# Kernel tuning notes

Measured on AMD Instinct MI355X. Metric: run time of the kernel, lower is better.

The kernel has to match this reference:

```python
import jax, jax.numpy as jnp
import numpy as np

EMBED_DIM = 1024
NUM_HEADS = 16
HEAD_DIM = EMBED_DIM // NUM_HEADS
LN_EPS = 1e-5


def setup_inputs() -> dict:
    key = jax.random.key(0)
    ks = jax.random.split(key, 5)
    N, L, C = 32, 577, EMBED_DIM
    x = jax.random.normal(ks[0], (N, L, C), dtype=jnp.float32)
    ln1_g = jnp.ones((C,), dtype=jnp.float32)
    ln1_b = jnp.zeros((C,), dtype=jnp.float32)
    w_in = jax.random.normal(ks[1], (3 * C, C), dtype=jnp.float32) * (C ** -0.5)
    b_in = jax.random.normal(ks[2], (3 * C,), dtype=jnp.float32) * 0.02
    w_out = jax.random.normal(ks[3], (C, C), dtype=jnp.float32) * (C ** -0.5)
    b_out = jax.random.normal(ks[4], (C,), dtype=jnp.float32) * 0.02
    return {"x": x, "ln1_g": ln1_g, "ln1_b": ln1_b, "w_in": w_in,
            "b_in": b_in, "w_out": w_out, "b_out": b_out}


def _layernorm(x, g, b):
    mu = jnp.mean(x, axis=-1, keepdims=True)
    var = jnp.mean(jnp.square(x - mu), axis=-1, keepdims=True)
    return (x - mu) * jax.lax.rsqrt(var + LN_EPS) * g + b


def reference(x, ln1_g, ln1_b, w_in, b_in, w_out, b_out):
    # ClearCLIP last block, attn_variant='qq', keep_residual=False, keep_ffn=False.
    N, L, C = x.shape
    H, D = NUM_HEADS, HEAD_DIM
    z = _layernorm(x, ln1_g, ln1_b)
    qkv = z @ w_in.T + b_in                      # (N, L, 3C)
    q, k, v = jnp.split(qkv, 3, axis=-1)
    k = q                                        # 'qq' self-self variant
    def heads(t):
        return t.reshape(N, L, H, D).transpose(0, 2, 1, 3)  # (N, H, L, D)
    q, k, v = heads(q), heads(k), heads(v)
    scale = 1.0 / np.sqrt(D).astype(np.float32)
    scores = jnp.einsum('nhld,nhsd->nhls', q, k) * scale    # (N, H, L, L)
    attn = jax.nn.softmax(scores, axis=-1)
    out = jnp.einsum('nhls,nhsd->nhld', attn, v)            # (N, H, L, D)
    out = out.transpose(0, 2, 1, 3).reshape(N, L, C)
    return out @ w_out.T + b_out                 # ls_1 = Identity, no residual/FFN
```

## Files before the change

kernel.cpp:

```cpp
#include <hip/hip_runtime.h>
#include <stdint.h>

typedef short bf16x8 __attribute__((ext_vector_type(8)));
typedef float f32x4 __attribute__((ext_vector_type(4)));
typedef unsigned int uint4v __attribute__((ext_vector_type(4)));
typedef unsigned short ushort4v __attribute__((ext_vector_type(4)));
typedef float float4v __attribute__((ext_vector_type(4)));

#define MROWS 18464
#define MPAD  18560
#define SEQ   577
#define CDIM  1024
#define SPAD  640
#define W1ELEMS (2048*1024)
#define W2ELEMS (1024*1024)
#define SQC 0.42466089f

__device__ __forceinline__ unsigned short f2bf(float f) {
  unsigned int u = __float_as_uint(f);
  u += 0x7fffu + ((u >> 16) & 1u);
  return (unsigned short)(u >> 16);
}

__device__ __forceinline__ void load_lds16(const void* g, void* lds) {
  __builtin_amdgcn_global_load_lds(
      (const __attribute__((address_space(1))) unsigned int*)(uint64_t)(uintptr_t)g,
      (__attribute__((address_space(3))) unsigned int*)(unsigned int)(uintptr_t)lds,
      16, 0, 0);
}

__global__ __launch_bounds__(256) void ln_kernel(const float* __restrict__ x,
                                                 const float* __restrict__ g,
                                                 const float* __restrict__ b,
                                                 unsigned short* __restrict__ z) {
  const int row = blockIdx.x;
  const int t = threadIdx.x;
  unsigned short* zp = z + (size_t)row * CDIM + t * 4;
  if (row >= MROWS) { *(ushort4v*)zp = (ushort4v)0; return; }
  const float4v v = *(const float4v*)(x + (size_t)row * CDIM + t * 4);
  float s  = v[0] + v[1] + v[2] + v[3];
  float ss = v[0]*v[0] + v[1]*v[1] + v[2]*v[2] + v[3]*v[3];
  #pragma unroll
  for (int off = 1; off < 64; off <<= 1) { s += __shfl_xor(s, off); ss += __shfl_xor(ss, off); }
  __shared__ float rs[4], rss[4];
  const int w = t >> 6, l = t & 63;
  if (l == 0) { rs[w] = s; rss[w] = ss; }
  __syncthreads();
  s = rs[0] + rs[1] + rs[2] + rs[3];
  ss = rss[0] + rss[1] + rss[2] + rss[3];
  const float mu = s * (1.0f / CDIM);
  const float var = ss * (1.0f / CDIM) - mu * mu;
  const float rstd = rsqrtf(var + 1e-5f);
  const float4v gv = *(const float4v*)(g + t * 4);
  const float4v bv = *(const float4v*)(b + t * 4);
  ushort4v o;
  #pragma unroll
  for (int j = 0; j < 4; ++j) o[j] = f2bf((v[j] - mu) * rstd * gv[j] + bv[j]);
  *(ushort4v*)zp = o;
}

__global__ __launch_bounds__(256) void conv_kernel(const float* __restrict__ w_in,
                                                   const float* __restrict__ w_out,
                                                   unsigned short* __restrict__ wqv,
                                                   unsigned short* __restrict__ wo,
                                                   unsigned short* __restrict__ vt) {
  const int idx = blockIdx.x * 256 + threadIdx.x;
  const int e = idx * 4;
  if (e < W1ELEMS) {
    const int row = e >> 10;
    const int srow = row < 1024 ? row : row + 1024;
    const float4v v = *(const float4v*)(w_in + (size_t)srow * 1024 + (e & 1023));
    ushort4v o;
    #pragma unroll
    for (int j = 0; j < 4; ++j) o[j] = f2bf(v[j]);
    *(ushort4v*)(wqv + e) = o;
  } else if (e < W1ELEMS + W2ELEMS) {
    const int e2 = e - W1ELEMS;
    const float4v v = *(const float4v*)(w_out + e2);
    ushort4v o;
    #pragma unroll
    for (int j = 0; j < 4; ++j) o[j] = f2bf(v[j]);
    *(ushort4v*)(wo + e2) = o;
  } else {
    const int pidx = idx - (W1ELEMS + W2ELEMS) / 4;
    const int ic = pidx >> 3, part = pidx & 7;
    *(uint4v*)(vt + (size_t)ic * SPAD + 576 + part * 8) = (uint4v)0u;
  }
}

template<int MODE>
__global__ __launch_bounds__(256) void gemm_kernel(const unsigned short* __restrict__ A,
                                                   const unsigned short* __restrict__ B,
                                                   const float* __restrict__ bias,
                                                   void* __restrict__ outp) {
  __shared__ char smem[98304];
  const int t = threadIdx.x;
  const int w = t >> 6, l = t & 63;
  const int L = (blockIdx.x & 7) * 145 + (blockIdx.x >> 3);
  const int p = L >> 3, c = L & 7;
  const int m0 = (MODE == 2) ? c * 128 : p * 128;
  const int n0 = (MODE == 2) ? p * 128 : c * 128;
  const int wr = w >> 1, wc = w & 1;
  const int g4 = (l >> 4) * 4;
  const int fr = l & 15;

  f32x4 acc[4][4];
  #pragma unroll
  for (int i = 0; i < 4; ++i)
    #pragma unroll
    for (int j = 0; j < 4; ++j) acc[i][j] = (f32x4)0.0f;

  const int srow = l >> 3;
  const int scol = ((((l & 7) * 16) ^ ((srow & 7) << 4)) >> 1);
  const int fb = (l >> 4) * 16;
  const int sw = (l & 7) << 4;

  const unsigned short* Ab = A + (size_t)(m0 + w * 32 + srow) * 1024 + scol;
  const unsigned short* Bb = B + (size_t)(n0 + w * 32 + srow) * 1024 + scol;

  #define STAGE(kt, slot)                                                        \
    {                                                                            \
      char* const base_ = smem + (slot) * 32768 + (w * 32) * 128;                \
      const int k0_ = (kt) * 64;                                                 \
      _Pragma("unroll")                                                          \
      for (int c2 = 0; c2 < 4; ++c2) {                                           \
        load_lds16(Ab + (size_t)(c2 * 8) * 1024 + k0_, base_ + c2 * 1024);       \
        load_lds16(Bb + (size_t)(c2 * 8) * 1024 + k0_, base_ + 16384 + c2 * 1024);\
      }                                                                          \
    }

  STAGE(0, 0)
  STAGE(1, 1)

  for (int kb = 0; kb < 16; ++kb) {
    if (kb < 15) { asm volatile("s_waitcnt vmcnt(8)" ::: "memory"); }
    else         { asm volatile("s_waitcnt vmcnt(0)" ::: "memory"); }
    __builtin_amdgcn_sched_barrier(0);
    __builtin_amdgcn_s_barrier();

    const char* Abuf = smem + (kb % 3) * 32768;
    const char* Bbuf = Abuf + 16384;
    #pragma unroll
    for (int kk = 0; kk < 2; ++kk) {
      bf16x8 af[4], bf[4];
      #pragma unroll
      for (int i = 0; i < 4; ++i)
        af[i] = *(const bf16x8*)(Abuf + (wr * 64 + i * 16 + fr) * 128 + ((kk * 64 + fb) ^ sw));
      #pragma unroll
      for (int j = 0; j < 4; ++j)
        bf[j] = *(const bf16x8*)(Bbuf + (wc * 64 + j * 16 + fr) * 128 + ((kk * 64 + fb) ^ sw));
      #pragma unroll
      for (int i = 0; i < 4; ++i)
        #pragma unroll
        for (int j = 0; j < 4; ++j)
          acc[i][j] = __builtin_amdgcn_mfma_f32_16x16x32_bf16(af[i], bf[j], acc[i][j], 0, 0, 0);
    }

    if (kb < 14) STAGE(kb + 2, (kb + 2) % 3)
  }
  #undef STAGE

  __syncthreads();

  if constexpr (MODE == 0) {
    unsigned short* sm = (unsigned short*)smem;
    float bcol[4];
    #pragma unroll
    for (int j = 0; j < 4; ++j) bcol[j] = bias[n0 + wc * 64 + j * 16 + fr];
    #pragma unroll
    for (int i = 0; i < 4; ++i)
      #pragma unroll
      for (int j = 0; j < 4; ++j)
        #pragma unroll
        for (int r = 0; r < 4; ++r)
          sm[(wr * 64 + i * 16 + g4 + r) * 136 + wc * 64 + j * 16 + fr] =
              f2bf((acc[i][j][r] + bcol[j]) * SQC);
    __syncthreads();
    #pragma unroll
    for (int it = 0; it < 8; ++it) {
      const int cid = it * 256 + t;
      const int row = cid >> 4, ch = cid & 15;
      *(uint4v*)((unsigned short*)outp + (size_t)(m0 + row) * 1024 + n0 + ch * 8) =
          *(const uint4v*)(sm + row * 136 + ch * 8);
    }
  } else if constexpr (MODE == 1) {
    float* smf = (float*)smem;
    float bcol[4];
    #pragma unroll
    for (int j = 0; j < 4; ++j) bcol[j] = bias[n0 + wc * 64 + j * 16 + fr];
    #pragma unroll
    for (int i = 0; i < 4; ++i)
      #pragma unroll
      for (int j = 0; j < 4; ++j)
        #pragma unroll
        for (int r = 0; r < 4; ++r)
          smf[(wr * 64 + i * 16 + g4 + r) * 132 + wc * 64 + j * 16 + fr] =
              acc[i][j][r] + bcol[j];
    __syncthreads();
    float* o = (float*)outp;
    #pragma unroll
    for (int it = 0; it < 16; ++it) {
      const int cid = it * 256 + t;
      const int row = cid >> 5, ch = cid & 31;
      const int grow = m0 + row;
      if (grow < MROWS)
        *(float4v*)(o + (size_t)grow * 1024 + n0 + ch * 4) =
            *(const float4v*)(smf + row * 132 + ch * 4);
    }
  } else {
    unsigned short* sm = (unsigned short*)smem;
    float brow[4][4];
    #pragma unroll
    for (int i = 0; i < 4; ++i)
      #pragma unroll
      for (int r = 0; r < 4; ++r) brow[i][r] = bias[m0 + wr * 64 + i * 16 + g4 + r];
    #pragma unroll
    for (int i = 0; i < 4; ++i)
      #pragma unroll
      for (int j = 0; j < 4; ++j)
        #pragma unroll
        for (int r = 0; r < 4; ++r)
          sm[(wr * 64 + i * 16 + g4 + r) * 136 + wc * 64 + j * 16 + fr] =
              f2bf(acc[i][j][r] + brow[i][r]);
    __syncthreads();
    unsigned short* o = (unsigned short*)outp;
    const int col = t & 127;
    const int rbase = t >> 7;
    const int token = n0 + col;
    if (token < MROWS) {
      const unsigned int nimg = (unsigned int)token / 577u;
      const int s = token - (int)(nimg * 577u);
      unsigned short* op = o + ((size_t)nimg * 1024 + m0 + rbase) * SPAD + s;
      const unsigned short* sp = sm + rbase * 136 + col;
      #pragma unroll 8
      for (int it = 0; it < 64; ++it)
        op[(size_t)it * 2 * SPAD] = sp[it * 2 * 136];
    }
  }
}

__global__ __launch_bounds__(256) void attn_kernel(const unsigned short* __restrict__ qbuf,
                                                   const unsigned short* __restrict__ vt,
                                                   unsigned short* __restrict__ out) {
  __shared__ char smem[32768];
  const int t = threadIdx.x, w = t >> 6, l = t & 63;
  const int g = l >> 4, fr = l & 15;
  const int bid = blockIdx.x;
  const int xcd = bid & 7, idx = bid >> 3;
  const int nhl = idx / 5;
  const int qb = idx - nhl * 5;
  const int nh = xcd * 64 + nhl;
  const int n = nh >> 4, h = nh & 15;
  const size_t rowbase = (size_t)n * SEQ;
  const int sw = (l & 7) << 4;

  bf16x8 bq[2][2];
  #pragma unroll
  for (int half = 0; half < 2; ++half) {
    const unsigned short* qp =
        qbuf + (rowbase + qb * 128 + half * 64 + w * 16 + fr) * 1024 + h * 64 + g * 8;
    bq[half][0] = *(const bf16x8*)qp;
    bq[half][1] = *(const bf16x8*)(qp + 32);
  }

  const int srow = l >> 3;
  const int scolE = ((((l & 7) * 16) ^ ((srow & 7) << 4)) >> 1);
  const unsigned short* ksrc = qbuf + (rowbase + w * 16 + srow) * 1024 + h * 64 + scolE;
  const unsigned short* vsrc = vt + ((size_t)nh * 64 + w * 16 + srow) * SPAD + scolE;

  f32x4 acc[2][4];
  #pragma unroll
  for (int half = 0; half < 2; ++half)
    #pragma unroll
    for (int cf = 0; cf < 4; ++cf) acc[half][cf] = (f32x4)0.0f;
  float l_run[2] = {0.0f, 0.0f};

  {
    char* kdst = smem + (w * 16) * 128;
    char* vdst = smem + 8192 + (w * 16) * 128;
    load_lds16(ksrc, kdst);
    load_lds16(ksrc + (size_t)8 * 1024, kdst + 1024);
    load_lds16(vsrc, vdst);
    load_lds16(vsrc + 8 * SPAD, vdst + 1024);
  }
  __syncthreads();

  for (int kb = 0; kb < 10; ++kb) {
    const int b = kb & 1;
    const char* kbuf = smem + b * 16384;
    const char* vbuf = kbuf + 8192;

    if (kb < 9) {
      char* kdst = smem + (b ^ 1) * 16384 + (w * 16) * 128;
      char* vdst = kdst + 8192;
      load_lds16(ksrc + (size_t)((kb + 1) * 64) * 1024, kdst);
      load_lds16(ksrc + (size_t)((kb + 1) * 64 + 8) * 1024, kdst + 1024);
      load_lds16(vsrc + (kb + 1) * 64, vdst);
      load_lds16(vsrc + 8 * SPAD + (kb + 1) * 64, vdst + 1024);
    }

    f32x4 s4[2][4];
    #pragma unroll
    for (int half = 0; half < 2; ++half)
      #pragma unroll
      for (int cf = 0; cf < 4; ++cf) s4[half][cf] = (f32x4)0.0f;
    #pragma unroll
    for (int kk = 0; kk < 2; ++kk)
      #pragma unroll
      for (int cf = 0; cf < 4; ++cf) {
        const bf16x8 af = *(const bf16x8*)(kbuf + (cf * 16 + fr) * 128 + ((kk * 64 + g * 16) ^ sw));
        s4[0][cf] = __builtin_amdgcn_mfma_f32_16x16x32_bf16(af, bq[0][kk], s4[0][cf], 0, 0, 0);
        s4[1][cf] = __builtin_amdgcn_mfma_f32_16x16x32_bf16(af, bq[1][kk], s4[1][cf], 0, 0, 0);
      }

    if (kb == 9) {
      #pragma unroll
      for (int half = 0; half < 2; ++half) {
        #pragma unroll
        for (int cf = 0; cf < 4; ++cf)
          #pragma unroll
          for (int r = 0; r < 4; ++r)
            if (cf != 0 || r != 0) s4[half][cf][r] = -__builtin_inff();
        s4[half][0][0] = (g == 0) ? s4[half][0][0] : -__builtin_inff();
      }
    }

    bf16x8 ap[2][2];
    #pragma unroll
    for (int half = 0; half < 2; ++half) {
      float sum = 0.0f;
      #pragma unroll
      for (int cf = 0; cf < 4; ++cf)
        #pragma unroll
        for (int r = 0; r < 4; ++r) {
          const float p = __builtin_amdgcn_exp2f(s4[half][cf][r]);
          s4[half][cf][r] = p;
          sum += p;
        }
      sum += __shfl_xor(sum, 16);
      sum += __shfl_xor(sum, 32);
      l_run[half] += sum;

      unsigned int pka[4], pkb[4];
      #pragma unroll
      for (int cf = 0; cf < 4; ++cf) {
        asm("v_cvt_pk_bf16_f32 %0, %1, %2" : "=v"(pka[cf]) : "v"(s4[half][cf][0]), "v"(s4[half][cf][1]));
        asm("v_cvt_pk_bf16_f32 %0, %1, %2" : "=v"(pkb[cf]) : "v"(s4[half][cf][2]), "v"(s4[half][cf][3]));
      }
      #pragma unroll
      for (int kk = 0; kk < 2; ++kk) {
        unsigned int a0 = pka[2 * kk], b0 = pka[2 * kk + 1];
        unsigned int a1 = pkb[2 * kk], b1 = pkb[2 * kk + 1];
        asm("v_permlane32_swap_b32 %0, %1" : "+v"(a0), "+v"(b0));
        asm("v_permlane16_swap_b32 %0, %1" : "+v"(a0), "+v"(b0));
        asm("v_permlane32_swap_b32 %0, %1" : "+v"(a1), "+v"(b1));
        asm("v_permlane16_swap_b32 %0, %1" : "+v"(a1), "+v"(b1));
        union { unsigned int i[4]; bf16x8 v; } u;
        u.i[0] = a0; u.i[1] = a1; u.i[2] = b0; u.i[3] = b1;
        ap[half][kk] = u.v;
      }
    }

    #pragma unroll
    for (int kk = 0; kk < 2; ++kk)
      #pragma unroll
      for (int cf = 0; cf < 4; ++cf) {
        const bf16x8 bv = *(const bf16x8*)(vbuf + (cf * 16 + fr) * 128 + ((kk * 64 + g * 16) ^ sw));
        acc[0][cf] = __builtin_amdgcn_mfma_f32_16x16x32_bf16(ap[0][kk], bv, acc[0][cf], 0, 0, 0);
        acc[1][cf] = __builtin_amdgcn_mfma_f32_16x16x32_bf16(ap[1][kk], bv, acc[1][cf], 0, 0, 0);
      }

    __syncthreads();
  }

  #pragma unroll
  for (int half = 0; half < 2; ++half) {
    const float rcp = 1.0f / l_run[half];
    #pragma unroll
    for (int r = 0; r < 4; ++r) {
      const float rr = __shfl(rcp, g * 4 + r);
      const int qg = qb * 128 + half * 64 + w * 16 + g * 4 + r;
      if (qg < SEQ) {
        #pragma unroll
        for (int cf = 0; cf < 4; ++cf)
          out[(rowbase + qg) * 1024 + h * 64 + cf * 16 + fr] = f2bf(acc[half][cf][r] * rr);
      }
    }
  }
}

extern "C" void kernel_launch(void* const* d_in, const int* in_sizes, int n_in,
                              void* d_out, int out_size, void* d_ws, size_t ws_size,
                              hipStream_t stream) {
  const float* x     = (const float*)d_in[0];
  const float* ln_g  = (const float*)d_in[1];
  const float* ln_b  = (const float*)d_in[2];
  const float* w_in  = (const float*)d_in[3];
  const float* b_in  = (const float*)d_in[4];
  const float* w_out = (const float*)d_in[5];
  const float* b_out = (const float*)d_in[6];

  unsigned short* z    = (unsigned short*)d_ws;
  unsigned short* qbuf = z + (size_t)MPAD * 1024;
  unsigned short* vt   = qbuf + (size_t)MPAD * 1024;
  unsigned short* wqv  = vt + (size_t)512 * 64 * SPAD;
  unsigned short* wo   = wqv + (size_t)2048 * 1024;

  ln_kernel<<<MPAD, 256, 0, stream>>>(x, ln_g, ln_b, z);
  conv_kernel<<<4096, 256, 0, stream>>>(w_in, w_out, wqv, wo, vt);
  gemm_kernel<0><<<1160, 256, 0, stream>>>(z, wqv, b_in, qbuf);
  gemm_kernel<2><<<1160, 256, 0, stream>>>(wqv + (size_t)1024 * 1024, z, b_in + 2048, vt);
  attn_kernel<<<2560, 256, 0, stream>>>(qbuf, vt, z);
  gemm_kernel<1><<<1160, 256, 0, stream>>>(z, wo, b_out, (float*)d_out);
}
```

Measured before the change: 286.4 us.

## Merge Q and V projections into one 256x256-tile GEMM with 512 threads

Replaces the 128x128 GEMM kernel with a 256x256-tile, 8-wave version using double-buffered LDS. The Q and V projections now run as a single launch, with the V half writing its transposed layout directly in the epilogue. Padded rows are dropped by clamping A-row addresses and guarding stores instead of zero-filling pad rows in layernorm. The larger tiles are meant to raise data reuse per block and cut launch count, but the grid shrinks to 584 and 292 blocks, which may fill the CUs poorly. The pipeline also drops from three LDS stages to two.

New measurement: 250.7 us. -12.5%, faster.

```diff
diff --git a/kernel.cpp b/kernel.cpp
--- a/kernel.cpp
+++ b/kernel.cpp
@@ -8,7 +8,6 @@
 typedef float float4v __attribute__((ext_vector_type(4)));
 
 #define MROWS 18464
-#define MPAD  18560
 #define SEQ   577
 #define CDIM  1024
 #define SPAD  640
@@ -35,8 +34,6 @@
                                                  unsigned short* __restrict__ z) {
   const int row = blockIdx.x;
   const int t = threadIdx.x;
-  unsigned short* zp = z + (size_t)row * CDIM + t * 4;
-  if (row >= MROWS) { *(ushort4v*)zp = (ushort4v)0; return; }
   const float4v v = *(const float4v*)(x + (size_t)row * CDIM + t * 4);
   float s  = v[0] + v[1] + v[2] + v[3];
   float ss = v[0]*v[0] + v[1]*v[1] + v[2]*v[2] + v[3]*v[3];
@@ -56,7 +53,7 @@
   ushort4v o;
   #pragma unroll
   for (int j = 0; j < 4; ++j) o[j] = f2bf((v[j] - mu) * rstd * gv[j] + bv[j]);
-  *(ushort4v*)zp = o;
+  *(ushort4v*)(z + (size_t)row * CDIM + t * 4) = o;
 }
 
 __global__ __launch_bounds__(256) void conv_kernel(const float* __restrict__ w_in,
@@ -89,152 +86,163 @@
 }
 
 template<int MODE>
-__global__ __launch_bounds__(256) void gemm_kernel(const unsigned short* __restrict__ A,
-                                                   const unsigned short* __restrict__ B,
-                                                   const float* __restrict__ bias,
-                                                   void* __restrict__ outp) {
-  __shared__ char smem[98304];
+__global__ __launch_bounds__(512, 2) void gemm256(const unsigned short* __restrict__ A,
+                                                  const unsigned short* __restrict__ B,
+                                                  const float* __restrict__ bias,
+                                                  void* __restrict__ outp,
+                                                  unsigned short* __restrict__ vtout) {
+  __shared__ char smem[131072];
   const int t = threadIdx.x;
   const int w = t >> 6, l = t & 63;
-  const int L = (blockIdx.x & 7) * 145 + (blockIdx.x >> 3);
-  const int p = L >> 3, c = L & 7;
-  const int m0 = (MODE == 2) ? c * 128 : p * 128;
-  const int n0 = (MODE == 2) ? p * 128 : c * 128;
-  const int wr = w >> 1, wc = w & 1;
+  int p, c;
+  if constexpr (MODE == 0) {
+    const int L = (blockIdx.x & 7) * 73 + (blockIdx.x >> 3);
+    p = L >> 3; c = L & 7;
+  } else {
+    const int xcd = blockIdx.x & 7, j = blockIdx.x >> 3;
+    const int L = (xcd < 4 ? xcd * 37 : 148 + (xcd - 4) * 36) + j;
+    p = L >> 2; c = L & 3;
+  }
+  const int m0 = p * 256;
+  const int n0 = c * 256;
+  const int wm = w >> 2, wn = w & 3;
   const int g4 = (l >> 4) * 4;
   const int fr = l & 15;
-
-  f32x4 acc[4][4];
-  #pragma unroll
-  for (int i = 0; i < 4; ++i)
+  const int fb = (l >> 4) * 16;
+  const int sw = (l & 7) << 4;
+
+  f32x4 acc[8][4];
+  #pragma unroll
+  for (int i = 0; i < 8; ++i)
     #pragma unroll
     for (int j = 0; j < 4; ++j) acc[i][j] = (f32x4)0.0f;
 
   const int srow = l >> 3;
   const int scol = ((((l & 7) * 16) ^ ((srow & 7) << 4)) >> 1);
-  const int fb = (l >> 4) * 16;
-  const int sw = (l & 7) << 4;
-
-  const unsigned short* Ab = A + (size_t)(m0 + w * 32 + srow) * 1024 + scol;
-  const unsigned short* Bb = B + (size_t)(n0 + w * 32 + srow) * 1024 + scol;
-
-  #define STAGE(kt, slot)                                                        \
-    {                                                                            \
-      char* const base_ = smem + (slot) * 32768 + (w * 32) * 128;                \
-      const int k0_ = (kt) * 64;                                                 \
-      _Pragma("unroll")                                                          \
-      for (int c2 = 0; c2 < 4; ++c2) {                                           \
-        load_lds16(Ab + (size_t)(c2 * 8) * 1024 + k0_, base_ + c2 * 1024);       \
-        load_lds16(Bb + (size_t)(c2 * 8) * 1024 + k0_, base_ + 16384 + c2 * 1024);\
-      }                                                                          \
-    }
-
-  STAGE(0, 0)
-  STAGE(1, 1)
+  const unsigned short* Ap[4];
+  const unsigned short* Bp[4];
+  #pragma unroll
+  for (int c2 = 0; c2 < 4; ++c2) {
+    int arow = m0 + w * 32 + c2 * 8 + srow;
+    if (arow > MROWS - 1) arow = MROWS - 1;
+    Ap[c2] = A + (size_t)arow * 1024 + scol;
+    Bp[c2] = B + (size_t)(n0 + w * 32 + c2 * 8 + srow) * 1024 + scol;
+  }
+
+  #define STG(kt, buf)                                                     \
+    {                                                                      \
+      char* const d_ = smem + (buf) * 65536 + w * 4096;                    \
+      const int k0_ = (kt) * 64;                                           \
+      _Pragma("unroll")                                                    \
+      for (int c2 = 0; c2 < 4; ++c2) {                                     \
+        load_lds16(Ap[c2] + k0_, d_ + c2 * 1024);                          \
+        load_lds16(Bp[c2] + k0_, d_ + 32768 + c2 * 1024);                  \
+      }                                                                    \
+    }
+
+  STG(0, 0)
+  __syncthreads();
 
   for (int kb = 0; kb < 16; ++kb) {
-    if (kb < 15) { asm volatile("s_waitcnt vmcnt(8)" ::: "memory"); }
-    else         { asm volatile("s_waitcnt vmcnt(0)" ::: "memory"); }
-    __builtin_amdgcn_sched_barrier(0);
-    __builtin_amdgcn_s_barrier();
-
-    const char* Abuf = smem + (kb % 3) * 32768;
-    const char* Bbuf = Abuf + 16384;
+    const int b = kb & 1;
+    if (kb < 15) STG(kb + 1, b ^ 1)
+    const char* Ab = smem + b * 65536;
+    const char* Bb = Ab + 32768;
     #pragma unroll
     for (int kk = 0; kk < 2; ++kk) {
-      bf16x8 af[4], bf[4];
-      #pragma unroll
-      for (int i = 0; i < 4; ++i)
-        af[i] = *(const bf16x8*)(Abuf + (wr * 64 + i * 16 + fr) * 128 + ((kk * 64 + fb) ^ sw));
+      bf16x8 af[8], bfr[4];
+      #pragma unroll
+      for (int i = 0; i < 8; ++i)
+        af[i] = *(const bf16x8*)(Ab + (wm * 128 + i * 16 + fr) * 128 + ((kk * 64 + fb) ^ sw));
       #pragma unroll
       for (int j = 0; j < 4; ++j)
-        bf[j] = *(const bf16x8*)(Bbuf + (wc * 64 + j * 16 + fr) * 128 + ((kk * 64 + fb) ^ sw));
-      #pragma unroll
-      for (int i = 0; i < 4; ++i)
+        bfr[j] = *(const bf16x8*)(Bb + (wn * 64 + j * 16 + fr) * 128 + ((kk * 64 + fb) ^ sw));
+      #pragma unroll
+      for (int i = 0; i < 8; ++i)
         #pragma unroll
         for (int j = 0; j < 4; ++j)
-          acc[i][j] = __builtin_amdgcn_mfma_f32_16x16x32_bf16(af[i], bf[j], acc[i][j], 0, 0, 0);
-    }
-
-    if (kb < 14) STAGE(kb + 2, (kb + 2) % 3)
-  }
-  #undef STAGE
-
-  __syncthreads();
+          acc[i][j] = __builtin_amdgcn_mfma_f32_16x16x32_bf16(af[i], bfr[j], acc[i][j], 0, 0, 0);
+    }
+    __syncthreads();
+  }
+  #undef STG
 
   if constexpr (MODE == 0) {
     unsigned short* sm = (unsigned short*)smem;
+    const bool isq = (n0 < 1024);
+    const float* bb = isq ? (bias + n0) : (bias + 1024 + n0);
+    const float scl = isq ? SQC : 1.0f;
     float bcol[4];
     #pragma unroll
-    for (int j = 0; j < 4; ++j) bcol[j] = bias[n0 + wc * 64 + j * 16 + fr];
-    #pragma unroll
-    for (int i = 0; i < 4; ++i)
-      #pragma unroll
-      for (int j = 0; j < 4; ++j)
-        #pragma unroll
-        for (int r = 0; r < 4; ++r)
-          sm[(wr * 64 + i * 16 + g4 + r) * 136 + wc * 64 + j * 16 + fr] =
-              f2bf((acc[i][j][r] + bcol[j]) * SQC);
-    __syncthreads();
-    #pragma unroll
-    for (int it = 0; it < 8; ++it) {
-      const int cid = it * 256 + t;
-      const int row = cid >> 4, ch = cid & 15;
-      *(uint4v*)((unsigned short*)outp + (size_t)(m0 + row) * 1024 + n0 + ch * 8) =
-          *(const uint4v*)(sm + row * 136 + ch * 8);
-    }
-  } else if constexpr (MODE == 1) {
+    for (int j = 0; j < 4; ++j) bcol[j] = bb[wn * 64 + j * 16 + fr];
+    for (int pass = 0; pass < 2; ++pass) {
+      if (wm == pass) {
+        #pragma unroll
+        for (int i = 0; i < 8; ++i)
+          #pragma unroll
+          for (int j = 0; j < 4; ++j)
+            #pragma unroll
+            for (int r = 0; r < 4; ++r)
+              sm[(i * 16 + g4 + r) * 264 + wn * 64 + j * 16 + fr] =
+                  f2bf((acc[i][j][r] + bcol[j]) * scl);
+      }
+      __syncthreads();
+      if (isq) {
+        unsigned short* o = (unsigned short*)outp;
+        #pragma unroll
+        for (int it = 0; it < 8; ++it) {
+          const int cid = it * 512 + t;
+          const int row = cid >> 5, ch = cid & 31;
+          const int grow = m0 + pass * 128 + row;
+          if (grow < MROWS)
+            *(uint4v*)(o + (size_t)grow * 1024 + n0 + ch * 8) =
+                *(const uint4v*)(sm + row * 264 + ch * 8);
+        }
+      } else {
+        const int rowloc = t & 127, chb = t >> 7;
+        const int token = m0 + pass * 128 + rowloc;
+        if (token < MROWS) {
+          const unsigned int nimg = (unsigned int)token / 577u;
+          const int s = token - (int)(nimg * 577u);
+          unsigned short* op =
+              vtout + ((size_t)nimg * 1024 + (n0 - 1024) + chb * 64) * SPAD + s;
+          const unsigned short* sp = sm + rowloc * 264 + chb * 64;
+          #pragma unroll 8
+          for (int it = 0; it < 64; ++it)
+            op[(size_t)it * SPAD] = sp[it];
+        }
+      }
+      __syncthreads();
+    }
+  } else {
     float* smf = (float*)smem;
     float bcol[4];
     #pragma unroll
-    for (int j = 0; j < 4; ++j) bcol[j] = bias[n0 + wc * 64 + j * 16 + fr];
-    #pragma unroll
-    for (int i = 0; i < 4; ++i)
-      #pragma unroll
-      for (int j = 0; j < 4; ++j)
-        #pragma unroll
-        for (int r = 0; r < 4; ++r)
-          smf[(wr * 64 + i * 16 + g4 + r) * 132 + wc * 64 + j * 16 + fr] =
-              acc[i][j][r] + bcol[j];
-    __syncthreads();
+    for (int j = 0; j < 4; ++j) bcol[j] = bias[n0 + wn * 64 + j * 16 + fr];
     float* o = (float*)outp;
-    #pragma unroll
-    for (int it = 0; it < 16; ++it) {
-      const int cid = it * 256 + t;
-      const int row = cid >> 5, ch = cid & 31;
-      const int grow = m0 + row;
-      if (grow < MROWS)
-        *(float4v*)(o + (size_t)grow * 1024 + n0 + ch * 4) =
-            *(const float4v*)(smf + row * 132 + ch * 4);
-    }
-  } else {
-    unsigned short* sm = (unsigned short*)smem;
-    float brow[4][4];
-    #pragma unroll
-    for (int i = 0; i < 4; ++i)
-      #pragma unroll
-      for (int r = 0; r < 4; ++r) brow[i][r] = bias[m0 + wr * 64 + i * 16 + g4 + r];
-    #pragma unroll
-    for (int i = 0; i < 4; ++i)
-      #pragma unroll
-      for (int j = 0; j < 4; ++j)
-        #pragma unroll
-        for (int r = 0; r < 4; ++r)
-          sm[(wr * 64 + i * 16 + g4 + r) * 136 + wc * 64 + j * 16 + fr] =
-              f2bf(acc[i][j][r] + brow[i][r]);
-    __syncthreads();
-    unsigned short* o = (unsigned short*)outp;
-    const int col = t & 127;
-    const int rbase = t >> 7;
-    const int token = n0 + col;
-    if (token < MROWS) {
-      const unsigned int nimg = (unsigned int)token / 577u;
-      const int s = token - (int)(nimg * 577u);
-      unsigned short* op = o + ((size_t)nimg * 1024 + m0 + rbase) * SPAD + s;
-      const unsigned short* sp = sm + rbase * 136 + col;
-      #pragma unroll 8
-      for (int it = 0; it < 64; ++it)
-        op[(size_t)it * 2 * SPAD] = sp[it * 2 * 136];
+    for (int q4 = 0; q4 < 4; ++q4) {
+      if (wm == (q4 >> 1)) {
+        const int i0 = (q4 & 1) * 4;
+        #pragma unroll
+        for (int i2 = 0; i2 < 4; ++i2)
+          #pragma unroll
+          for (int j = 0; j < 4; ++j)
+            #pragma unroll
+            for (int r = 0; r < 4; ++r)
+              smf[(i2 * 16 + g4 + r) * 260 + wn * 64 + j * 16 + fr] =
+                  acc[i0 + i2][j][r] + bcol[j];
+      }
+      __syncthreads();
+      #pragma unroll
+      for (int it = 0; it < 8; ++it) {
+        const int cid = it * 512 + t;
+        const int row = cid >> 6, ch = cid & 63;
+        const int grow = m0 + q4 * 64 + row;
+        if (grow < MROWS)
+          *(float4v*)(o + (size_t)grow * 1024 + n0 + ch * 4) =
+              *(const float4v*)(smf + row * 260 + ch * 4);
+      }
+      __syncthreads();
     }
   }
 }
@@ -333,9 +341,9 @@
       for (int cf = 0; cf < 4; ++cf)
         #pragma unroll
         for (int r = 0; r < 4; ++r) {
-          const float p = __builtin_amdgcn_exp2f(s4[half][cf][r]);
-          s4[half][cf][r] = p;
-          sum += p;
+          const float p2 = __builtin_amdgcn_exp2f(s4[half][cf][r]);
+          s4[half][cf][r] = p2;
+          sum += p2;
         }
       sum += __shfl_xor(sum, 16);
       sum += __shfl_xor(sum, 32);
@@ -401,15 +409,14 @@
   const float* b_out = (const float*)d_in[6];
 
   unsigned short* z    = (unsigned short*)d_ws;
-  unsigned short* qbuf = z + (size_t)MPAD * 1024;
-  unsigned short* vt   = qbuf + (size_t)MPAD * 1024;
+  unsigned short* qbuf = z + (size_t)MROWS * 1024;
+  unsigned short* vt   = qbuf + (size_t)MROWS * 1024;
   unsigned short* wqv  = vt + (size_t)512 * 64 * SPAD;
   unsigned short* wo   = wqv + (size_t)2048 * 1024;
 
-  ln_kernel<<<MPAD, 256, 0, stream>>>(x, ln_g, ln_b, z);
+  ln_kernel<<<MROWS, 256, 0, stream>>>(x, ln_g, ln_b, z);
   conv_kernel<<<4096, 256, 0, stream>>>(w_in, w_out, wqv, wo, vt);
-  gemm_kernel<0><<<1160, 256, 0, stream>>>(z, wqv, b_in, qbuf);
-  gemm_kernel<2><<<1160, 256, 0, stream>>>(wqv + (size_t)1024 * 1024, z, b_in + 2048, vt);
+  gemm256<0><<<584, 512, 0, stream>>>(z, wqv, b_in, qbuf, vt);
   attn_kernel<<<2560, 256, 0, stream>>>(qbuf, vt, z);
-  gemm_kernel<1><<<1160, 256, 0, stream>>>(z, wo, b_out, (float*)d_out);
-}
+  gemm256<1><<<292, 512, 0, stream>>>(z, wo, b_out, d_out, nullptr);
+}
```
